# Performance work log

Measured on AMD Instinct MI355X. Metric: run time of the kernel, lower is better.

Reference implementation:

```python
import jax, jax.numpy as jnp
import numpy as np

B, C, H, W = 4, 96, 64, 64
N_STATE, DT_RANK, K = 16, 6, 3


def _layernorm(x, g, b, eps=1e-5):
    m = jnp.mean(x, axis=-1, keepdims=True)
    v = jnp.mean((x - m) ** 2, axis=-1, keepdims=True)
    return (x - m) / jnp.sqrt(v + eps) * g + b


def _grid_sample(img, gx, gy):
    # F.grid_sample: bilinear, align_corners=True, zeros padding; gx,gy in [-1,1], [B,Ho,Wo]
    Bc, Cc, Hi, Wi = img.shape
    fx = (gx + 1.0) * 0.5 * (Wi - 1)
    fy = (gy + 1.0) * 0.5 * (Hi - 1)
    x0 = jnp.floor(fx)
    y0 = jnp.floor(fy)
    wx1 = fx - x0
    wy1 = fy - y0

    def tap(ix, iy, w):
        valid = ((ix >= 0) & (ix < Wi) & (iy >= 0) & (iy < Hi)).astype(img.dtype)
        ic = jnp.clip(ix, 0, Wi - 1).astype(jnp.int32)
        jc = jnp.clip(iy, 0, Hi - 1).astype(jnp.int32)
        v = jax.vmap(lambda im, yy, xx: im[:, yy, xx])(img, jc, ic)  # [B,C,Ho,Wo]
        return v * (w * valid)[:, None, :, :]

    return (tap(x0, y0, (1 - wx1) * (1 - wy1)) + tap(x0 + 1, y0, wx1 * (1 - wy1))
            + tap(x0, y0 + 1, (1 - wx1) * wy1) + tap(x0 + 1, y0 + 1, wx1 * wy1))


def _resize_bilinear(img, Ho, Wo):
    # torch F.interpolate(mode='bilinear', align_corners=False)
    Bc, Cc, Hi, Wi = img.shape

    def src(n_out, n_in):
        s = jnp.maximum((jnp.arange(n_out, dtype=img.dtype) + 0.5) * (n_in / n_out) - 0.5, 0.0)
        i0 = jnp.floor(s).astype(jnp.int32)
        i1 = jnp.minimum(i0 + 1, n_in - 1)
        return i0, i1, s - i0

    y0, y1, wy = src(Ho, Hi)
    x0, x1, wx = src(Wo, Wi)
    row = img[:, :, y0, :] * (1 - wy)[None, None, :, None] + img[:, :, y1, :] * wy[None, None, :, None]
    return row[:, :, :, x0] * (1 - wx) + row[:, :, :, x1] * wx


def _conv_offset(x, conv1_w, conv1_b, ca1_w, ca1_b, ca2_w, ca2_b, ln_g, ln_b, conv2_w):
    Bc, Cc = x.shape[:2]
    p = conv1_w.shape[-1] // 2
    x1 = jax.lax.conv_general_dilated(
        x, conv1_w, (1, 1), [(p, p), (p, p)],
        dimension_numbers=("NCHW", "OIHW", "NCHW"), feature_group_count=Cc
    ) + conv1_b[None, :, None, None]
    xc = jnp.mean(x, axis=(2, 3))  # adaptive_avg_pool2d -> (1,1)
    hid = jax.nn.gelu(xc @ ca1_w.T + ca1_b, approximate=False)
    ca = jax.nn.sigmoid(hid @ ca2_w.T + ca2_b)
    x1 = x1 * ca[:, :, None, None]
    xn = _layernorm(jnp.transpose(x1, (0, 2, 3, 1)), ln_g, ln_b)
    xg = jax.nn.gelu(jnp.transpose(xn, (0, 3, 1, 2)), approximate=False)
    return jnp.einsum("bchw,oc->bohw", xg, conv2_w[:, :, 0, 0])


def _deformable(x, rpe_table, conv1_w, conv1_b, ca1_w, ca1_b, ca2_w, ca2_b, ln_g, ln_b, conv2_w):
    Bc, Cc, Hc, Wc = x.shape
    L = Hc * Wc
    off = _conv_offset(x, conv1_w, conv1_b, ca1_w, ca1_b, ca2_w, ca2_b, ln_g, ln_b, conv2_w)
    offset = off[:, :2]
    de = off[:, 2]
    rng = jnp.array([1.0 / (Hc - 1.0), 1.0 / (Wc - 1.0)], off.dtype).reshape(1, 2, 1, 1)
    offset = jnp.transpose(jnp.tanh(offset) * rng, (0, 2, 3, 1))  # [B,H,W,2] (dy,dx)
    ry = (jnp.linspace(0.5, Hc - 0.5, Hc) / (Hc - 1.0)) * 2.0 - 1.0
    rx = (jnp.linspace(0.5, Wc - 0.5, Wc) / (Wc - 1.0)) * 2.0 - 1.0
    ref = jnp.stack(jnp.meshgrid(ry, rx, indexing="ij"), -1)  # [H,W,2] (y,x)
    pos = offset + ref[None]
    de_index = jnp.tanh(de).reshape(Bc, L)
    path_ref = (jnp.linspace(0.5, L - 0.5, L) / (L - 1.0)) * 2.0 - 1.0
    path_pos = de_index + path_ref[None]
    x_sampled = _grid_sample(x, pos[..., 1], pos[..., 0])
    rpe = jnp.broadcast_to(rpe_table[None], (Bc,) + rpe_table.shape)
    rpe_bias = _resize_bilinear(rpe, Hc, Wc)
    ky = (jnp.linspace(0.0, float(Hc), Hc) / (Hc - 1.0)) * 2.0 - 1.0
    kx = (jnp.linspace(0.0, float(Wc), Wc) / (Wc - 1.0)) * 2.0 - 1.0
    key_grid = jnp.stack(jnp.meshgrid(ky, kx, indexing="ij"), -1)
    disp = (key_grid[None] - pos) * 0.5
    pos_bias = _grid_sample(rpe_bias, disp[..., 1], disp[..., 0])
    xd = (x_sampled + pos_bias).reshape(Bc, Cc, L)
    indices = jnp.argsort(path_pos, axis=-1)  # topk(k=N, largest=False) == ascending argsort
    xs2 = jnp.take_along_axis(xd, indices[:, None, :], axis=2)
    return xs2, indices


def _selective_scan(u, delta, A, Bs, Cs, Dv, delta_bias):
    Bc, KD, L = u.shape
    Kk = Bs.shape[1]
    Dd = KD // Kk
    Ns = A.shape[1]
    delta = jax.nn.softplus(delta + delta_bias[None, :, None])
    dt4 = jnp.moveaxis(delta.reshape(Bc, Kk, Dd, L), 3, 0)
    u4 = jnp.moveaxis(u.reshape(Bc, Kk, Dd, L), 3, 0)
    Bt = jnp.moveaxis(Bs, 3, 0)
    Ct = jnp.moveaxis(Cs, 3, 0)
    A3 = A.reshape(Kk, Dd, Ns)

    @jax.checkpoint
    def step(h, inp):
        dt, ut, bt, ct = inp  # [B,K,D],[B,K,D],[B,K,N],[B,K,N]
        h = jnp.exp(dt[..., None] * A3) * h + (dt * ut)[..., None] * bt[:, :, None, :]
        return h, jnp.einsum("bkdn,bkn->bkd", h, ct)

    h0 = jnp.zeros((Bc, Kk, Dd, Ns), u.dtype)
    _, ys = jax.lax.scan(step, h0, (dt4, u4, Bt, Ct))
    ys = jnp.moveaxis(ys, 0, 3).reshape(Bc, KD, L)
    return ys + u * Dv[None, :, None]


def _forward(x, x_proj_weight, dt_projs_weight, dt_projs_bias, A_logs, Ds_param,
             conv1_w, conv1_b, ca1_w, ca1_b, ca2_w, ca2_b, ln_g, ln_b, conv2_w, rpe_table):
    Bc, Dd, Hc, Wc = x.shape
    L = Hc * Wc
    Kk, _, R = dt_projs_weight.shape
    Ns = A_logs.shape[1]
    xs0 = x.reshape(Bc, Dd, L)
    xs2, indices = _deformable(x, rpe_table, conv1_w, conv1_b, ca1_w, ca1_b, ca2_w, ca2_b, ln_g, ln_b, conv2_w)
    xs = jnp.stack([xs0, xs0[..., ::-1], xs2], axis=1)  # [B,3,D,L]
    x_dbl = jnp.einsum("bkdl,kcd->bkcl", xs, x_proj_weight)
    dts, Bs, Cs = jnp.split(x_dbl, [R, R + Ns], axis=2)
    dts = jnp.einsum("bkrl,kdr->bkdl", dts, dt_projs_weight)
    A = -jnp.exp(A_logs)
    ys = _selective_scan(xs.reshape(Bc, Kk * Dd, L), dts.reshape(Bc, Kk * Dd, L),
                         A, Bs, Cs, Ds_param, dt_projs_bias.reshape(-1))
    ys = ys.reshape(Bc, Kk, Dd, L)
    inv = jnp.argsort(indices, axis=-1)  # inverse permutation (DeformableLayerReverse)
    y2 = jnp.take_along_axis(ys[:, 2], inv[:, None, :], axis=2)
    y = (ys[:, 0] + ys[:, 1][..., ::-1] + y2) / 3.0
    return jnp.transpose(y, (0, 2, 1)).reshape(Bc, Hc, Wc, Dd)


def setup_inputs():
    key = jax.random.key(0)
    ks = jax.random.split(key, 12)
    f = jnp.float32
    return {
        "x": jax.random.normal(ks[0], (B, C, H, W), f),
        "x_proj_weight": jax.random.normal(ks[1], (K, DT_RANK + 2 * N_STATE, C), f) * 0.05,
        "dt_projs_weight": jax.random.normal(ks[2], (K, C, DT_RANK), f) * 0.05,
        "dt_projs_bias": jax.random.normal(ks[3], (K, C), f) * 0.1,
        "A_logs": jnp.tile(jnp.log(jnp.arange(1, N_STATE + 1, dtype=f))[None, :], (K * C, 1)),
        "Ds_param": jnp.ones((K * C,), f),
        "conv1_w": jax.random.normal(ks[4], (C, 1, 9, 9), f) * 0.05,
        "conv1_b": jnp.zeros((C,), f),
        "ca1_w": jax.random.normal(ks[5], (C // 16, C), f) * 0.1,
        "ca1_b": jnp.zeros((C // 16,), f),
        "ca2_w": jax.random.normal(ks[6], (C, C // 16), f) * 0.1,
        "ca2_b": jnp.zeros((C,), f),
        "ln_g": jnp.ones((C,), f),
        "ln_b": jnp.zeros((C,), f),
        "conv2_w": jax.random.normal(ks[7], (3, C, 1, 1), f) * 0.05,
        "rpe_table": jax.random.normal(ks[8], (C, 7, 7), f) * 0.01,
    }


def reference(x, x_proj_weight, dt_projs_weight, dt_projs_bias, A_logs, Ds_param,
              conv1_w, conv1_b, ca1_w, ca1_b, ca2_w, ca2_b, ln_g, ln_b, conv2_w, rpe_table):
    return _forward(x, x_proj_weight, dt_projs_weight, dt_projs_bias, A_logs, Ds_param,
                    conv1_w, conv1_b, ca1_w, ca1_b, ca2_w, ca2_b, ln_g, ln_b, conv2_w, rpe_table)
```

## Files before the change

### kernel.cpp

```cpp
#include <hip/hip_runtime.h>

#define BB 4
#define CC 96
#define HH 64
#define WW 64
#define LL 4096
#define KK 3
#define RR 6
#define NN 16

__device__ __forceinline__ float geluf(float x){
    return 0.5f * x * (1.0f + erff(x * 0.70710678118654752f));
}
__device__ __forceinline__ float softplusf(float x){
    return fmaxf(x, 0.0f) + log1pf(expf(-fabsf(x)));
}
__device__ __forceinline__ float sigmoidf(float x){
    return 1.0f / (1.0f + expf(-x));
}

__global__ __launch_bounds__(256) void k_mean(const float* __restrict__ x, float* __restrict__ xc){
    int bc = blockIdx.x;
    const float* p = x + (size_t)bc * LL;
    float s = 0.f;
    for (int i = threadIdx.x; i < LL; i += 256) s += p[i];
    __shared__ float red[256];
    red[threadIdx.x] = s; __syncthreads();
    for (int st = 128; st > 0; st >>= 1){
        if (threadIdx.x < st) red[threadIdx.x] += red[threadIdx.x + st];
        __syncthreads();
    }
    if (threadIdx.x == 0) xc[bc] = red[0] * (1.0f / LL);
}

__global__ __launch_bounds__(128) void k_ca(const float* __restrict__ xc,
                     const float* __restrict__ w1, const float* __restrict__ b1,
                     const float* __restrict__ w2, const float* __restrict__ b2,
                     float* __restrict__ ca){
    int b = blockIdx.x;
    int t = threadIdx.x;
    __shared__ float hid[CC/16];
    if (t < CC/16){
        float a = b1[t];
        for (int d = 0; d < CC; d++) a += w1[t*CC + d] * xc[b*CC + d];
        hid[t] = geluf(a);
    }
    __syncthreads();
    if (t < CC){
        float a = b2[t];
        #pragma unroll
        for (int i = 0; i < CC/16; i++) a += w2[t*(CC/16) + i] * hid[i];
        ca[b*CC + t] = sigmoidf(a);
    }
}

__global__ __launch_bounds__(256) void k_conv(const float* __restrict__ x, const float* __restrict__ w,
                       const float* __restrict__ bias, const float* __restrict__ ca,
                       float* __restrict__ x1){
    int gid = blockIdx.x * 256 + threadIdx.x;
    int l = gid & (LL-1); int bc = gid >> 12;
    int c = bc % CC; int b = bc / CC;
    int h = l >> 6, wq = l & 63;
    const float* xp = x + (size_t)bc * LL;
    const float* wp = w + c * 81;
    float acc = 0.f;
    #pragma unroll
    for (int ky = 0; ky < 9; ky++){
        int yy = h + ky - 4;
        if (yy < 0 || yy >= HH) continue;
        #pragma unroll
        for (int kx = 0; kx < 9; kx++){
            int xx = wq + kx - 4;
            if (xx < 0 || xx >= WW) continue;
            acc += xp[yy*WW + xx] * wp[ky*9 + kx];
        }
    }
    x1[gid] = (acc + bias[c]) * ca[b*CC + c];
}

__global__ __launch_bounds__(256) void k_rpe(const float* __restrict__ t, float* __restrict__ out){
    int gid = blockIdx.x * 256 + threadIdx.x;
    int l = gid & (LL-1); int c = gid >> 12;
    int h = l >> 6, w = l & 63;
    float sy = fmaxf((h + 0.5f) * (7.0f/64.0f) - 0.5f, 0.f);
    float sx = fmaxf((w + 0.5f) * (7.0f/64.0f) - 0.5f, 0.f);
    int y0 = (int)floorf(sy); int x0 = (int)floorf(sx);
    float wy = sy - (float)y0, wx = sx - (float)x0;
    int y1 = min(y0 + 1, 6), x1i = min(x0 + 1, 6);
    const float* tp = t + c * 49;
    float r0 = tp[y0*7 + x0] * (1.f - wy) + tp[y1*7 + x0] * wy;
    float r1 = tp[y0*7 + x1i] * (1.f - wy) + tp[y1*7 + x1i] * wy;
    out[gid] = r0 * (1.f - wx) + r1 * wx;
}

__global__ __launch_bounds__(256) void k_off(const float* __restrict__ x1,
                      const float* __restrict__ g, const float* __restrict__ bta,
                      const float* __restrict__ w2,
                      float* __restrict__ posy, float* __restrict__ posx, float* __restrict__ path){
    int blk = blockIdx.x;
    int ltile = blk & 63; int b = blk >> 6;
    int lane = threadIdx.x & 63;
    int wg = threadIdx.x >> 6;
    int l = ltile * 64 + lane;
    const float* p = x1 + (size_t)b * CC * LL + l;
    float v[24];
    float s = 0.f, ss = 0.f;
    #pragma unroll
    for (int j = 0; j < 24; j++){
        float t = p[(size_t)(wg*24 + j) * LL];
        v[j] = t; s += t; ss += t*t;
    }
    __shared__ float ls[4][64], lss[4][64];
    ls[wg][lane] = s; lss[wg][lane] = ss;
    __syncthreads();
    s  = ls[0][lane]  + ls[1][lane]  + ls[2][lane]  + ls[3][lane];
    ss = lss[0][lane] + lss[1][lane] + lss[2][lane] + lss[3][lane];
    float m = s * (1.0f/CC);
    float rstd = rsqrtf(ss*(1.0f/CC) - m*m + 1e-5f);
    float a0 = 0.f, a1 = 0.f, a2 = 0.f;
    #pragma unroll
    for (int j = 0; j < 24; j++){
        int c = wg*24 + j;
        float xn = (v[j]-m)*rstd*g[c] + bta[c];
        float xg = geluf(xn);
        a0 = fmaf(w2[c],      xg, a0);
        a1 = fmaf(w2[CC+c],   xg, a1);
        a2 = fmaf(w2[2*CC+c], xg, a2);
    }
    __shared__ float la[3][4][64];
    la[0][wg][lane] = a0; la[1][wg][lane] = a1; la[2][wg][lane] = a2;
    __syncthreads();
    if (wg < 3){
        float a = la[wg][0][lane] + la[wg][1][lane] + la[wg][2][lane] + la[wg][3][lane];
        int h = l >> 6, w = l & 63;
        if (wg == 0)      posy[b*LL + l] = tanhf(a)*(1.0f/63.0f) + ((2*h+1)*(1.0f/63.0f) - 1.0f);
        else if (wg == 1) posx[b*LL + l] = tanhf(a)*(1.0f/63.0f) + ((2*w+1)*(1.0f/63.0f) - 1.0f);
        else              path[b*LL + l] = tanhf(a) + ((l + 0.5f)*(2.0f/4095.0f) - 1.0f);
    }
}

typedef unsigned long long u64s;
__device__ __forceinline__ u64s shflx64(u64s x, int m){
    int lo = __shfl_xor((int)(unsigned)x, m);
    int hi = __shfl_xor((int)(unsigned)(x >> 32), m);
    return ((u64s)(unsigned)hi << 32) | (unsigned)lo;
}
__device__ __forceinline__ void cex(u64s& a, u64s& b, bool up){
    u64s mn = a < b ? a : b;
    u64s mx = a < b ? b : a;
    a = up ? mn : mx;
    b = up ? mx : mn;
}
__global__ __launch_bounds__(1024) void k_sort(const float* __restrict__ path,
                                               int* __restrict__ idx, int* __restrict__ inv){
    int b = blockIdx.x;
    int t = threadIdx.x;
    __shared__ u64s lds[LL];
    u64s v[4];
    #pragma unroll
    for (int r = 0; r < 4; r++){
        int e = t*4 + r;
        unsigned u = __float_as_uint(path[b*LL + e]);
        u ^= (u >> 31) ? 0xFFFFFFFFu : 0x80000000u;
        v[r] = ((u64s)u << 32) | (unsigned)e;
    }
    for (int kk = 2; kk <= LL; kk <<= 1){
        for (int j = kk >> 1; j > 0; j >>= 1){
            if (j >= 256){
                __syncthreads();
                #pragma unroll
                for (int r = 0; r < 4; r++) lds[t*4 + r] = v[r];
                __syncthreads();
                #pragma unroll
                for (int r = 0; r < 4; r++){
                    int e = t*4 + r;
                    u64s pv = lds[e ^ j];
                    bool up    = ((e & kk) == 0);
                    bool lower = ((e & j) == 0);
                    u64s mn = v[r] < pv ? v[r] : pv;
                    u64s mx = v[r] < pv ? pv : v[r];
                    v[r] = (up == lower) ? mn : mx;
                }
            } else if (j >= 4){
                int m = j >> 2;
                #pragma unroll
                for (int r = 0; r < 4; r++){
                    u64s pv = shflx64(v[r], m);
                    bool up    = (((t*4 + r) & kk) == 0);
                    bool lower = ((t & m) == 0);
                    u64s mn = v[r] < pv ? v[r] : pv;
                    u64s mx = v[r] < pv ? pv : v[r];
                    v[r] = (up == lower) ? mn : mx;
                }
            } else if (j == 2){
                bool up = (((t*4) & kk) == 0);
                cex(v[0], v[2], up);
                cex(v[1], v[3], up);
            } else {
                if (kk == 2){
                    cex(v[0], v[1], true);
                    cex(v[2], v[3], false);
                } else {
                    bool up = (((t*4) & kk) == 0);
                    cex(v[0], v[1], up);
                    cex(v[2], v[3], up);
                }
            }
        }
    }
    #pragma unroll
    for (int r = 0; r < 4; r++){
        int e = t*4 + r;
        int id = (int)(unsigned)(v[r] & 0xFFFFFFFFu);
        idx[b*LL + e] = id;
        inv[b*LL + id] = e;
    }
}

__device__ __forceinline__ float bilin0(const float* __restrict__ img, float gx, float gy){
    float fx = (gx + 1.f) * 31.5f;
    float fy = (gy + 1.f) * 31.5f;
    float x0f = floorf(fx), y0f = floorf(fy);
    float wx = fx - x0f, wy = fy - y0f;
    int x0 = (int)x0f, y0 = (int)y0f;
    float acc = 0.f;
    bool vx0 = (x0 >= 0) & (x0 < WW), vx1 = (x0+1 >= 0) & (x0+1 < WW);
    bool vy0 = (y0 >= 0) & (y0 < HH), vy1 = (y0+1 >= 0) & (y0+1 < HH);
    if (vy0 & vx0) acc += img[y0*WW + x0]       * (1.f-wx) * (1.f-wy);
    if (vy0 & vx1) acc += img[y0*WW + x0+1]     * wx       * (1.f-wy);
    if (vy1 & vx0) acc += img[(y0+1)*WW + x0]   * (1.f-wx) * wy;
    if (vy1 & vx1) acc += img[(y0+1)*WW + x0+1] * wx       * wy;
    return acc;
}

__global__ __launch_bounds__(256) void k_sample(const float* __restrict__ x, const float* __restrict__ rpe,
                         const float* __restrict__ posy, const float* __restrict__ posx,
                         float* __restrict__ xd){
    int gid = blockIdx.x * 256 + threadIdx.x;
    int l = gid & (LL-1); int bc = gid >> 12;
    int b = bc / CC; int c = bc % CC;
    float gy = posy[b*LL + l], gx = posx[b*LL + l];
    float v = bilin0(x + (size_t)bc * LL, gx, gy);
    int h = l >> 6, w = l & 63;
    float ky = h * (128.0f/3969.0f) - 1.0f;
    float kx = w * (128.0f/3969.0f) - 1.0f;
    float v2 = bilin0(rpe + (size_t)c * LL, (kx - gx) * 0.5f, (ky - gy) * 0.5f);
    xd[gid] = v + v2;
}

__global__ __launch_bounds__(192, 1) void k_proj(const float* __restrict__ x, const float* __restrict__ xd,
    const int* __restrict__ indices, const float* __restrict__ xpw, const float* __restrict__ dtw,
    const float* __restrict__ dtb, float* __restrict__ u2, float* __restrict__ dt,
    float* __restrict__ Bst, float* __restrict__ Cst){
    int blk = blockIdx.x;
    int ltile = blk & 63; int bk = blk >> 6;
    int k = bk % KK; int b = bk / KK;
    int lane = threadIdx.x & 63;
    int w = threadIdx.x >> 6;
    const float* __restrict__ Wk = xpw + k*38*CC;
    int l = ltile * 64 + lane;
    int srcl = (k == 0) ? l : (k == 1 ? (LL-1-l) : indices[b*LL + l]);
    const float* xp = (k == 2 ? xd : x) + (size_t)b * CC * LL + srcl;

    __shared__ float vsh[CC*64];
    #pragma unroll
    for (int j = 0; j < 32; j++){
        int d = w*32 + j;
        vsh[d*64 + lane] = xp[(size_t)d * LL];
    }
    __syncthreads();

    if (w == 0){
        float acc[RR];
        #pragma unroll
        for (int i = 0; i < RR; i++) acc[i] = 0.f;
        for (int d = 0; d < CC; d++){
            float vv = vsh[d*64 + lane];
            #pragma unroll
            for (int i = 0; i < RR; i++) acc[i] = fmaf(Wk[i*CC + d], vv, acc[i]);
        }
        const float* __restrict__ Dw = dtw + k*CC*RR;
        const float* __restrict__ Db = dtb + k*CC;
        float* dtp = dt + (size_t)bk * CC * LL + l;
        #pragma unroll 8
        for (int d = 0; d < CC; d++){
            float sdt = Db[d];
            #pragma unroll
            for (int r = 0; r < RR; r++) sdt = fmaf(acc[r], Dw[d*RR + r], sdt);
            dtp[(size_t)d * LL] = softplusf(sdt);
        }
    } else if (w == 1){
        float acc[NN];
        #pragma unroll
        for (int i = 0; i < NN; i++) acc[i] = 0.f;
        for (int d = 0; d < CC; d++){
            float vv = vsh[d*64 + lane];
            #pragma unroll
            for (int i = 0; i < NN; i++) acc[i] = fmaf(Wk[(RR + i)*CC + d], vv, acc[i]);
        }
        size_t base = ((size_t)bk * LL + l) * NN;
        #pragma unroll
        for (int q = 0; q < 4; q++){
            float4 o; o.x = acc[q*4]; o.y = acc[q*4+1]; o.z = acc[q*4+2]; o.w = acc[q*4+3];
            *(float4*)(Bst + base + q*4) = o;
        }
    } else {
        float acc[NN];
        #pragma unroll
        for (int i = 0; i < NN; i++) acc[i] = 0.f;
        for (int d = 0; d < CC; d++){
            float vv = vsh[d*64 + lane];
            #pragma unroll
            for (int i = 0; i < NN; i++) acc[i] = fmaf(Wk[(RR + NN + i)*CC + d], vv, acc[i]);
        }
        size_t base = ((size_t)bk * LL + l) * NN;
        #pragma unroll
        for (int q = 0; q < 4; q++){
            float4 o; o.x = acc[q*4]; o.y = acc[q*4+1]; o.z = acc[q*4+2]; o.w = acc[q*4+3];
            *(float4*)(Cst + base + q*4) = o;
        }
        if (k == 2){
            float* up = u2 + (size_t)b * CC * LL + l;
            #pragma unroll 8
            for (int d = 0; d < CC; d++) up[(size_t)d * LL] = vsh[d*64 + lane];
        }
    }
}

#define SEG 128
#define TL 32
#define SROW 17
#define DROW 36
template<int KIND>
__device__ __forceinline__ void scan_body(int b, int d, const float* __restrict__ usrc,
    const float* __restrict__ dt, const float* __restrict__ Bst, const float* __restrict__ Cst,
    const float* __restrict__ Alog, const float* __restrict__ Ds, float* __restrict__ ys,
    float* sA, float* sB, float* sdt){
    int bk = b * KK + KIND;
    int tid = threadIdx.x;
    int ng = tid & 3;
    int seg = tid >> 2;
    int t0 = seg * TL;

    const float4 A4 = *(const float4*)(Alog + (KIND*CC + d)*NN + 4*ng);
    float A[4] = { -__expf(A4.x), -__expf(A4.y), -__expf(A4.z), -__expf(A4.w) };
    float Dv = Ds[KIND*CC + d];

    const float* dtp = dt + ((size_t)bk * CC + d) * LL + t0;
    const float* ub = (KIND == 1)
        ? usrc + ((size_t)b*CC + d) * LL + (LL-4-t0)
        : usrc + ((size_t)b*CC + d) * LL + t0;
    const float* Bp = Bst + ((size_t)bk * LL + t0) * NN + 4*ng;
    const float* Cp = Cst + ((size_t)bk * LL + t0) * NN + 4*ng;
    float* yp = ys + ((size_t)bk * CC + d) * LL + t0;

    float Ap[4] = {1.f,1.f,1.f,1.f}, h[4] = {0.f,0.f,0.f,0.f};
    for (int t = 0; t < TL; t += 4){
        float4 dq = *(const float4*)(dtp + t);
        float4 uq = (KIND == 1) ? *(const float4*)(ub - t) : *(const float4*)(ub + t);
        float dd[4] = {dq.x, dq.y, dq.z, dq.w};
        float uu[4];
        if (KIND == 1){ uu[0]=uq.w; uu[1]=uq.z; uu[2]=uq.y; uu[3]=uq.x; }
        else          { uu[0]=uq.x; uu[1]=uq.y; uu[2]=uq.z; uu[3]=uq.w; }
        if (ng == 0) *(float4*)(sdt + seg*DROW + t) = dq;
        #pragma unroll
        for (int i = 0; i < 4; i++){
            float4 Bq = *(const float4*)(Bp + (t+i)*NN);
            float du = dd[i] * uu[i];
            float bb[4] = {Bq.x, Bq.y, Bq.z, Bq.w};
            #pragma unroll
            for (int j = 0; j < 4; j++){
                float a = __expf(dd[i] * A[j]);
                Ap[j] *= a;
                h[j] = fmaf(a, h[j], du * bb[j]);
            }
        }
    }

    #pragma unroll
    for (int j = 0; j < 4; j++){
        sA[seg*SROW + 4*ng + j] = Ap[j];
        sB[seg*SROW + 4*ng + j] = h[j];
    }
    __syncthreads();
    {
        int wv = tid >> 6;
        int lane = tid & 63;
        #pragma unroll
        for (int nn = 0; nn < 2; nn++){
            int n = 2*wv + nn;
            float a1 = sA[(2*lane)*SROW + n],   b1 = sB[(2*lane)*SROW + n];
            float a2 = sA[(2*lane+1)*SROW + n], b2 = sB[(2*lane+1)*SROW + n];
            float ca = a1 * a2;
            float cb = fmaf(a2, b1, b2);
            #pragma unroll
            for (int off = 1; off < 64; off <<= 1){
                float ta = __shfl_up(ca, off);
                float tb = __shfl_up(cb, off);
                if (lane >= off){
                    cb = fmaf(ca, tb, cb);
                    ca *= ta;
                }
            }
            float cb_prev = __shfl_up(cb, 1);
            if (lane == 0) cb_prev = 0.f;
            sA[(2*lane)*SROW + n]   = cb_prev;
            sA[(2*lane+1)*SROW + n] = fmaf(a1, cb_prev, b1);
        }
    }
    __syncthreads();
    float hc[4];
    #pragma unroll
    for (int j = 0; j < 4; j++) hc[j] = sA[seg*SROW + 4*ng + j];

    for (int t = 0; t < TL; t += 4){
        float4 dq = *(const float4*)(sdt + seg*DROW + t);
        float4 uq = (KIND == 1) ? *(const float4*)(ub - t) : *(const float4*)(ub + t);
        float dd[4] = {dq.x, dq.y, dq.z, dq.w};
        float uu[4];
        if (KIND == 1){ uu[0]=uq.w; uu[1]=uq.z; uu[2]=uq.y; uu[3]=uq.x; }
        else          { uu[0]=uq.x; uu[1]=uq.y; uu[2]=uq.z; uu[3]=uq.w; }
        float yo[4];
        #pragma unroll
        for (int i = 0; i < 4; i++){
            float4 Bq = *(const float4*)(Bp + (t+i)*NN);
            float4 Cq = *(const float4*)(Cp + (t+i)*NN);
            float du = dd[i] * uu[i];
            float bb[4] = {Bq.x, Bq.y, Bq.z, Bq.w};
            float cc[4] = {Cq.x, Cq.y, Cq.z, Cq.w};
            float p = 0.f;
            #pragma unroll
            for (int j = 0; j < 4; j++){
                float a = __expf(dd[i] * A[j]);
                hc[j] = fmaf(a, hc[j], du * bb[j]);
                p = fmaf(hc[j], cc[j], p);
            }
            p += __shfl_xor(p, 1);
            p += __shfl_xor(p, 2);
            yo[i] = fmaf(uu[i], Dv, p);
        }
        if (ng == 0){
            float4 o; o.x = yo[0]; o.y = yo[1]; o.z = yo[2]; o.w = yo[3];
            *(float4*)(yp + t) = o;
        }
    }
}

__global__ __launch_bounds__(512) void k_scan_all(const float* __restrict__ x, const float* __restrict__ u2,
    const float* __restrict__ dt, const float* __restrict__ Bst, const float* __restrict__ Cst,
    const float* __restrict__ Alog, const float* __restrict__ Ds, float* __restrict__ ys){
    __shared__ float sA[SEG*SROW];
    __shared__ float sB[SEG*SROW];
    __shared__ float sdt[SEG*DROW];
    int blk = blockIdx.x;
    int k = blk / (BB*CC);
    int r = blk % (BB*CC);
    int d = r % CC; int b = r / CC;
    if (k == 0)      scan_body<0>(b, d, x,  dt, Bst, Cst, Alog, Ds, ys, sA, sB, sdt);
    else if (k == 1) scan_body<1>(b, d, x,  dt, Bst, Cst, Alog, Ds, ys, sA, sB, sdt);
    else             scan_body<2>(b, d, u2, dt, Bst, Cst, Alog, Ds, ys, sA, sB, sdt);
}

__global__ __launch_bounds__(256) void k_comb(const float* __restrict__ ys, const int* __restrict__ inv,
                                              float* __restrict__ out){
    int tile = blockIdx.x & 63; int b = blockIdx.x >> 6;
    int l0 = tile * 64;
    __shared__ float t0[CC * 65];
    __shared__ int invs[64];
    if (threadIdx.x < 64) invs[threadIdx.x] = inv[b*LL + l0 + threadIdx.x];
    __syncthreads();
    const float* y0p = ys + (size_t)(b*KK + 0) * CC * LL;
    const float* y1p = ys + (size_t)(b*KK + 1) * CC * LL;
    const float* y2p = ys + (size_t)(b*KK + 2) * CC * LL;
    for (int it = 0; it < 24; it++){
        int e = it * 256 + threadIdx.x;
        int li = e & 63; int c = e >> 6;
        int l = l0 + li;
        float v = y0p[(size_t)c*LL + l] + y1p[(size_t)c*LL + (LL-1-l)] + y2p[(size_t)c*LL + invs[li]];
        t0[c*65 + li] = v * (1.0f/3.0f);
    }
    __syncthreads();
    for (int it = 0; it < 24; it++){
        int e = it * 256 + threadIdx.x;
        int c = e % CC; int li = e / CC;
        out[((size_t)b*LL + l0 + li) * CC + c] = t0[c*65 + li];
    }
}

extern "C" void kernel_launch(void* const* d_in, const int* in_sizes, int n_in,
                              void* d_out, int out_size, void* d_ws, size_t ws_size,
                              hipStream_t stream){
    const float* x    = (const float*)d_in[0];
    const float* xpw  = (const float*)d_in[1];
    const float* dtw  = (const float*)d_in[2];
    const float* dtb  = (const float*)d_in[3];
    const float* Alog = (const float*)d_in[4];
    const float* Ds   = (const float*)d_in[5];
    const float* c1w  = (const float*)d_in[6];
    const float* c1b  = (const float*)d_in[7];
    const float* ca1w = (const float*)d_in[8];
    const float* ca1b = (const float*)d_in[9];
    const float* ca2w = (const float*)d_in[10];
    const float* ca2b = (const float*)d_in[11];
    const float* lng  = (const float*)d_in[12];
    const float* lnb  = (const float*)d_in[13];
    const float* c2w  = (const float*)d_in[14];
    const float* rpet = (const float*)d_in[15];
    float* out = (float*)d_out;

    float* ws   = (float*)d_ws;
    float* xc   = ws;
    float* ca   = xc + 384;
    float* x1   = ca + 384;
    float* rpe  = x1 + (size_t)BB*CC*LL;
    float* posy = rpe + (size_t)CC*LL;
    float* posx = posy + (size_t)BB*LL;
    float* path = posx + (size_t)BB*LL;
    float* xd   = path + (size_t)BB*LL;
    int*   idx  = (int*)(xd + (size_t)BB*CC*LL);
    int*   inv  = idx + (size_t)BB*LL;
    float* u2   = (float*)(inv + (size_t)BB*LL);
    float* dtA  = u2 + (size_t)BB*CC*LL;
    float* Bst  = dtA + (size_t)BB*KK*CC*LL;
    float* Cst  = Bst + (size_t)BB*KK*LL*NN;
    float* ysA  = Cst + (size_t)BB*KK*LL*NN;

    k_mean  <<<BB*CC, 256, 0, stream>>>(x, xc);
    k_ca    <<<BB, 128, 0, stream>>>(xc, ca1w, ca1b, ca2w, ca2b, ca);
    k_conv  <<<(BB*CC*LL)/256, 256, 0, stream>>>(x, c1w, c1b, ca, x1);
    k_rpe   <<<(CC*LL)/256, 256, 0, stream>>>(rpet, rpe);
    k_off   <<<BB*64, 256, 0, stream>>>(x1, lng, lnb, c2w, posy, posx, path);
    k_sort  <<<BB, 1024, 0, stream>>>(path, idx, inv);
    k_sample<<<(BB*CC*LL)/256, 256, 0, stream>>>(x, rpe, posy, posx, xd);
    k_proj  <<<BB*KK*64, 192, 0, stream>>>(x, xd, idx, xpw, dtw, dtb, u2, dtA, Bst, Cst);
    k_scan_all<<<KK*BB*CC, 512, 0, stream>>>(x, u2, dtA, Bst, Cst, Alog, Ds, ysA);
    k_comb  <<<BB*64, 256, 0, stream>>>(ysA, inv, out);
}
```

Before: 351.9 us.

## Merge sort with sampling kernel and avoid rescan via cumulative-dt correction

The sort and grid-sample kernels are merged into one launch, so the single-block-per-batch bitonic sort runs alongside the sampling blocks instead of serialising with them. The chunked selective scan now computes the local output during the first pass and stores prefix sums of dt. The second pass then only adds a correction term exp(A*cumdt)*h_carry·C, with no recurrence and no reloading of B, u and dt. This trades extra exp2 work and extra shared memory in the correction pass for the removed recurrence, and exp of a long cumulative dt may underflow differently from the stepwise product.

```diff
diff --git a/kernel.cpp b/kernel.cpp
--- a/kernel.cpp
+++ b/kernel.cpp
@@ -139,84 +139,6 @@
     }
 }
 
-typedef unsigned long long u64s;
-__device__ __forceinline__ u64s shflx64(u64s x, int m){
-    int lo = __shfl_xor((int)(unsigned)x, m);
-    int hi = __shfl_xor((int)(unsigned)(x >> 32), m);
-    return ((u64s)(unsigned)hi << 32) | (unsigned)lo;
-}
-__device__ __forceinline__ void cex(u64s& a, u64s& b, bool up){
-    u64s mn = a < b ? a : b;
-    u64s mx = a < b ? b : a;
-    a = up ? mn : mx;
-    b = up ? mx : mn;
-}
-__global__ __launch_bounds__(1024) void k_sort(const float* __restrict__ path,
-                                               int* __restrict__ idx, int* __restrict__ inv){
-    int b = blockIdx.x;
-    int t = threadIdx.x;
-    __shared__ u64s lds[LL];
-    u64s v[4];
-    #pragma unroll
-    for (int r = 0; r < 4; r++){
-        int e = t*4 + r;
-        unsigned u = __float_as_uint(path[b*LL + e]);
-        u ^= (u >> 31) ? 0xFFFFFFFFu : 0x80000000u;
-        v[r] = ((u64s)u << 32) | (unsigned)e;
-    }
-    for (int kk = 2; kk <= LL; kk <<= 1){
-        for (int j = kk >> 1; j > 0; j >>= 1){
-            if (j >= 256){
-                __syncthreads();
-                #pragma unroll
-                for (int r = 0; r < 4; r++) lds[t*4 + r] = v[r];
-                __syncthreads();
-                #pragma unroll
-                for (int r = 0; r < 4; r++){
-                    int e = t*4 + r;
-                    u64s pv = lds[e ^ j];
-                    bool up    = ((e & kk) == 0);
-                    bool lower = ((e & j) == 0);
-                    u64s mn = v[r] < pv ? v[r] : pv;
-                    u64s mx = v[r] < pv ? pv : v[r];
-                    v[r] = (up == lower) ? mn : mx;
-                }
-            } else if (j >= 4){
-                int m = j >> 2;
-                #pragma unroll
-                for (int r = 0; r < 4; r++){
-                    u64s pv = shflx64(v[r], m);
-                    bool up    = (((t*4 + r) & kk) == 0);
-                    bool lower = ((t & m) == 0);
-                    u64s mn = v[r] < pv ? v[r] : pv;
-                    u64s mx = v[r] < pv ? pv : v[r];
-                    v[r] = (up == lower) ? mn : mx;
-                }
-            } else if (j == 2){
-                bool up = (((t*4) & kk) == 0);
-                cex(v[0], v[2], up);
-                cex(v[1], v[3], up);
-            } else {
-                if (kk == 2){
-                    cex(v[0], v[1], true);
-                    cex(v[2], v[3], false);
-                } else {
-                    bool up = (((t*4) & kk) == 0);
-                    cex(v[0], v[1], up);
-                    cex(v[2], v[3], up);
-                }
-            }
-        }
-    }
-    #pragma unroll
-    for (int r = 0; r < 4; r++){
-        int e = t*4 + r;
-        int id = (int)(unsigned)(v[r] & 0xFFFFFFFFu);
-        idx[b*LL + e] = id;
-        inv[b*LL + id] = e;
-    }
-}
-
 __device__ __forceinline__ float bilin0(const float* __restrict__ img, float gx, float gy){
     float fx = (gx + 1.f) * 31.5f;
     float fy = (gy + 1.f) * 31.5f;
@@ -233,19 +155,99 @@
     return acc;
 }
 
-__global__ __launch_bounds__(256) void k_sample(const float* __restrict__ x, const float* __restrict__ rpe,
-                         const float* __restrict__ posy, const float* __restrict__ posx,
-                         float* __restrict__ xd){
-    int gid = blockIdx.x * 256 + threadIdx.x;
-    int l = gid & (LL-1); int bc = gid >> 12;
-    int b = bc / CC; int c = bc % CC;
-    float gy = posy[b*LL + l], gx = posx[b*LL + l];
-    float v = bilin0(x + (size_t)bc * LL, gx, gy);
-    int h = l >> 6, w = l & 63;
-    float ky = h * (128.0f/3969.0f) - 1.0f;
-    float kx = w * (128.0f/3969.0f) - 1.0f;
-    float v2 = bilin0(rpe + (size_t)c * LL, (kx - gx) * 0.5f, (ky - gy) * 0.5f);
-    xd[gid] = v + v2;
+typedef unsigned long long u64s;
+__device__ __forceinline__ u64s shflx64(u64s x, int m){
+    int lo = __shfl_xor((int)(unsigned)x, m);
+    int hi = __shfl_xor((int)(unsigned)(x >> 32), m);
+    return ((u64s)(unsigned)hi << 32) | (unsigned)lo;
+}
+__device__ __forceinline__ void cex(u64s& a, u64s& b, bool up){
+    u64s mn = a < b ? a : b;
+    u64s mx = a < b ? b : a;
+    a = up ? mn : mx;
+    b = up ? mx : mn;
+}
+__global__ __launch_bounds__(1024) void k_sortsample(
+        const float* __restrict__ path, int* __restrict__ idx, int* __restrict__ inv,
+        const float* __restrict__ x, const float* __restrict__ rpe,
+        const float* __restrict__ posy, const float* __restrict__ posx,
+        float* __restrict__ xd){
+    int blk = blockIdx.x;
+    if (blk < BB){
+        int b = blk;
+        int t = threadIdx.x;
+        __shared__ u64s lds[LL];
+        u64s v[4];
+        #pragma unroll
+        for (int r = 0; r < 4; r++){
+            int e = t*4 + r;
+            unsigned u = __float_as_uint(path[b*LL + e]);
+            u ^= (u >> 31) ? 0xFFFFFFFFu : 0x80000000u;
+            v[r] = ((u64s)u << 32) | (unsigned)e;
+        }
+        for (int kk = 2; kk <= LL; kk <<= 1){
+            for (int j = kk >> 1; j > 0; j >>= 1){
+                if (j >= 256){
+                    __syncthreads();
+                    #pragma unroll
+                    for (int r = 0; r < 4; r++) lds[t*4 + r] = v[r];
+                    __syncthreads();
+                    #pragma unroll
+                    for (int r = 0; r < 4; r++){
+                        int e = t*4 + r;
+                        u64s pv = lds[e ^ j];
+                        bool up    = ((e & kk) == 0);
+                        bool lower = ((e & j) == 0);
+                        u64s mn = v[r] < pv ? v[r] : pv;
+                        u64s mx = v[r] < pv ? pv : v[r];
+                        v[r] = (up == lower) ? mn : mx;
+                    }
+                } else if (j >= 4){
+                    int m = j >> 2;
+                    #pragma unroll
+                    for (int r = 0; r < 4; r++){
+                        u64s pv = shflx64(v[r], m);
+                        bool up    = (((t*4 + r) & kk) == 0);
+                        bool lower = ((t & m) == 0);
+                        u64s mn = v[r] < pv ? v[r] : pv;
+                        u64s mx = v[r] < pv ? pv : v[r];
+                        v[r] = (up == lower) ? mn : mx;
+                    }
+                } else if (j == 2){
+                    bool up = (((t*4) & kk) == 0);
+                    cex(v[0], v[2], up);
+                    cex(v[1], v[3], up);
+                } else {
+                    if (kk == 2){
+                        cex(v[0], v[1], true);
+                        cex(v[2], v[3], false);
+                    } else {
+                        bool up = (((t*4) & kk) == 0);
+                        cex(v[0], v[1], up);
+                        cex(v[2], v[3], up);
+                    }
+                }
+            }
+        }
+        #pragma unroll
+        for (int r = 0; r < 4; r++){
+            int e = t*4 + r;
+            int id = (int)(unsigned)(v[r] & 0xFFFFFFFFu);
+            idx[b*LL + e] = id;
+            inv[b*LL + id] = e;
+        }
+    } else {
+        int gid = (blk - BB) * 1024 + threadIdx.x;
+        int l = gid & (LL-1); int bc = gid >> 12;
+        int b = bc / CC; int c = bc % CC;
+        float gy = posy[b*LL + l], gx = posx[b*LL + l];
+        float v = bilin0(x + (size_t)bc * LL, gx, gy);
+        int h = l >> 6, w = l & 63;
+        float ky = h * (128.0f/3969.0f) - 1.0f;
+        float kx = w * (128.0f/3969.0f) - 1.0f;
+        float v2 = bilin0(rpe + (size_t)c * LL, (kx - gx) * 0.5f, (ky - gy) * 0.5f);
+        xd[gid] = v + v2;
+    }
 }
 
 __global__ __launch_bounds__(192, 1) void k_proj(const float* __restrict__ x, const float* __restrict__ xd,
@@ -330,12 +332,12 @@
 #define SEG 128
 #define TL 32
 #define SROW 17
-#define DROW 36
+#define XROW 36
 template<int KIND>
 __device__ __forceinline__ void scan_body(int b, int d, const float* __restrict__ usrc,
     const float* __restrict__ dt, const float* __restrict__ Bst, const float* __restrict__ Cst,
     const float* __restrict__ Alog, const float* __restrict__ Ds, float* __restrict__ ys,
-    float* sA, float* sB, float* sdt){
+    float* sA, float* sB, float* sS, float* yl){
     int bk = b * KK + KIND;
     int tid = threadIdx.x;
     int ng = tid & 3;
@@ -343,7 +345,8 @@
     int t0 = seg * TL;
 
     const float4 A4 = *(const float4*)(Alog + (KIND*CC + d)*NN + 4*ng);
-    float A[4] = { -__expf(A4.x), -__expf(A4.y), -__expf(A4.z), -__expf(A4.w) };
+    const float L2E = 1.4426950408889634f;
+    float A2[4] = { -__expf(A4.x)*L2E, -__expf(A4.y)*L2E, -__expf(A4.z)*L2E, -__expf(A4.w)*L2E };
     float Dv = Ds[KIND*CC + d];
 
     const float* dtp = dt + ((size_t)bk * CC + d) * LL + t0;
@@ -354,32 +357,49 @@
     const float* Cp = Cst + ((size_t)bk * LL + t0) * NN + 4*ng;
     float* yp = ys + ((size_t)bk * CC + d) * LL + t0;
 
-    float Ap[4] = {1.f,1.f,1.f,1.f}, h[4] = {0.f,0.f,0.f,0.f};
+    float h[4] = {0.f,0.f,0.f,0.f};
+    float S = 0.f;
     for (int t = 0; t < TL; t += 4){
         float4 dq = *(const float4*)(dtp + t);
         float4 uq = (KIND == 1) ? *(const float4*)(ub - t) : *(const float4*)(ub + t);
+        float4 Bq[4], Cq[4];
+        #pragma unroll
+        for (int i = 0; i < 4; i++){
+            Bq[i] = *(const float4*)(Bp + (t+i)*NN);
+            Cq[i] = *(const float4*)(Cp + (t+i)*NN);
+        }
         float dd[4] = {dq.x, dq.y, dq.z, dq.w};
         float uu[4];
         if (KIND == 1){ uu[0]=uq.w; uu[1]=uq.z; uu[2]=uq.y; uu[3]=uq.x; }
         else          { uu[0]=uq.x; uu[1]=uq.y; uu[2]=uq.z; uu[3]=uq.w; }
-        if (ng == 0) *(float4*)(sdt + seg*DROW + t) = dq;
+        float sv[4], pv[4];
         #pragma unroll
         for (int i = 0; i < 4; i++){
-            float4 Bq = *(const float4*)(Bp + (t+i)*NN);
             float du = dd[i] * uu[i];
-            float bb[4] = {Bq.x, Bq.y, Bq.z, Bq.w};
+            float bb[4] = {Bq[i].x, Bq[i].y, Bq[i].z, Bq[i].w};
+            float cc[4] = {Cq[i].x, Cq[i].y, Cq[i].z, Cq[i].w};
+            float p = 0.f;
             #pragma unroll
             for (int j = 0; j < 4; j++){
-                float a = __expf(dd[i] * A[j]);
-                Ap[j] *= a;
+                float a = exp2f(dd[i] * A2[j]);
                 h[j] = fmaf(a, h[j], du * bb[j]);
+                p = fmaf(h[j], cc[j], p);
             }
+            S += dd[i];
+            sv[i] = S;
+            p += __shfl_xor(p, 1);
+            p += __shfl_xor(p, 2);
+            pv[i] = fmaf(uu[i], Dv, p);
+        }
+        if (ng == 0){
+            *(float4*)(sS + seg*XROW + t) = make_float4(sv[0], sv[1], sv[2], sv[3]);
+            *(float4*)(yl + seg*XROW + t) = make_float4(pv[0], pv[1], pv[2], pv[3]);
         }
     }
 
     #pragma unroll
     for (int j = 0; j < 4; j++){
-        sA[seg*SROW + 4*ng + j] = Ap[j];
+        sA[seg*SROW + 4*ng + j] = exp2f(A2[j] * S);
         sB[seg*SROW + 4*ng + j] = h[j];
     }
     __syncthreads();
@@ -414,33 +434,28 @@
     for (int j = 0; j < 4; j++) hc[j] = sA[seg*SROW + 4*ng + j];
 
     for (int t = 0; t < TL; t += 4){
-        float4 dq = *(const float4*)(sdt + seg*DROW + t);
-        float4 uq = (KIND == 1) ? *(const float4*)(ub - t) : *(const float4*)(ub + t);
-        float dd[4] = {dq.x, dq.y, dq.z, dq.w};
-        float uu[4];
-        if (KIND == 1){ uu[0]=uq.w; uu[1]=uq.z; uu[2]=uq.y; uu[3]=uq.x; }
-        else          { uu[0]=uq.x; uu[1]=uq.y; uu[2]=uq.z; uu[3]=uq.w; }
+        float4 sq = *(const float4*)(sS + seg*XROW + t);
+        float4 Cq[4];
+        #pragma unroll
+        for (int i = 0; i < 4; i++) Cq[i] = *(const float4*)(Cp + (t+i)*NN);
+        float sv[4] = {sq.x, sq.y, sq.z, sq.w};
         float yo[4];
         #pragma unroll
         for (int i = 0; i < 4; i++){
-            float4 Bq = *(const float4*)(Bp + (t+i)*NN);
-            float4 Cq = *(const float4*)(Cp + (t+i)*NN);
-            float du = dd[i] * uu[i];
-            float bb[4] = {Bq.x, Bq.y, Bq.z, Bq.w};
-            float cc[4] = {Cq.x, Cq.y, Cq.z, Cq.w};
-            float p = 0.f;
+            float cc[4] = {Cq[i].x, Cq[i].y, Cq[i].z, Cq[i].w};
+            float corr = 0.f;
             #pragma unroll
             for (int j = 0; j < 4; j++){
-                float a = __expf(dd[i] * A[j]);
-                hc[j] = fmaf(a, hc[j], du * bb[j]);
-                p = fmaf(hc[j], cc[j], p);
+                float P = exp2f(sv[i] * A2[j]);
+                corr = fmaf(P * hc[j], cc[j], corr);
             }
-            p += __shfl_xor(p, 1);
-            p += __shfl_xor(p, 2);
-            yo[i] = fmaf(uu[i], Dv, p);
+            corr += __shfl_xor(corr, 1);
+            corr += __shfl_xor(corr, 2);
+            yo[i] = corr;
         }
         if (ng == 0){
-            float4 o; o.x = yo[0]; o.y = yo[1]; o.z = yo[2]; o.w = yo[3];
+            float4 ylq = *(const float4*)(yl + seg*XROW + t);
+            float4 o = make_float4(ylq.x + yo[0], ylq.y + yo[1], ylq.z + yo[2], ylq.w + yo[3]);
             *(float4*)(yp + t) = o;
         }
     }
@@ -451,14 +466,15 @@
     const float* __restrict__ Alog, const float* __restrict__ Ds, float* __restrict__ ys){
     __shared__ float sA[SEG*SROW];
     __shared__ float sB[SEG*SROW];
-    __shared__ float sdt[SEG*DROW];
+    __shared__ float sS[SEG*XROW];
+    __shared__ float yl[SEG*XROW];
     int blk = blockIdx.x;
     int k = blk / (BB*CC);
     int r = blk % (BB*CC);
     int d = r % CC; int b = r / CC;
-    if (k == 0)      scan_body<0>(b, d, x,  dt, Bst, Cst, Alog, Ds, ys, sA, sB, sdt);
-    else if (k == 1) scan_body<1>(b, d, x,  dt, Bst, Cst, Alog, Ds, ys, sA, sB, sdt);
-    else             scan_body<2>(b, d, u2, dt, Bst, Cst, Alog, Ds, ys, sA, sB, sdt);
+    if (k == 0)      scan_body<0>(b, d, x,  dt, Bst, Cst, Alog, Ds, ys, sA, sB, sS, yl);
+    else if (k == 1) scan_body<1>(b, d, x,  dt, Bst, Cst, Alog, Ds, ys, sA, sB, sS, yl);
+    else             scan_body<2>(b, d, u2, dt, Bst, Cst, Alog, Ds, ys, sA, sB, sS, yl);
 }
 
 __global__ __launch_bounds__(256) void k_comb(const float* __restrict__ ys, const int* __restrict__ inv,
@@ -530,8 +546,7 @@
     k_conv  <<<(BB*CC*LL)/256, 256, 0, stream>>>(x, c1w, c1b, ca, x1);
     k_rpe   <<<(CC*LL)/256, 256, 0, stream>>>(rpet, rpe);
     k_off   <<<BB*64, 256, 0, stream>>>(x1, lng, lnb, c2w, posy, posx, path);
-    k_sort  <<<BB, 1024, 0, stream>>>(path, idx, inv);
-    k_sample<<<(BB*CC*LL)/256, 256, 0, stream>>>(x, rpe, posy, posx, xd);
+    k_sortsample<<<BB + (BB*CC*LL)/1024, 1024, 0, stream>>>(path, idx, inv, x, rpe, posy, posx, xd);
     k_proj  <<<BB*KK*64, 192, 0, stream>>>(x, xd, idx, xpw, dtw, dtb, u2, dtA, Bst, Cst);
     k_scan_all<<<KK*BB*CC, 512, 0, stream>>>(x, u2, dtA, Bst, Cst, Alog, Ds, ysA);
     k_comb  <<<BB*64, 256, 0, stream>>>(ysA, inv, out);
```

After: 331.5 us. -5.8%, faster.
